# Kernel optimization log

Hardware: AMD Instinct MI355X
Metric: run time of the kernel (lower is better)

## Reference

```python
import jax, jax.numpy as jnp
import numpy as np

S, B, NC = 16, 8, 5
D, H, DH = 256, 16, 16
PS, IMG = 7, 28
P = (IMG // PS) ** 2  # 16 patches
L = 2
PD = PS * PS * 1  # 49
EF, EFT = 4, 0.5
DFT = int(EFT * D)


def layernorm(x, g, b, eps=1e-5):
    m = x.mean(-1, keepdims=True)
    v = ((x - m) ** 2).mean(-1, keepdims=True)
    return (x - m) / jnp.sqrt(v + eps) * g + b


def patchify(x):
    # 's b c (h p1) (w p2) -> s b (h w) (p1 p2 c)'
    s, bb, c, hh, ww = x.shape
    h, w = hh // PS, ww // PS
    x = x.reshape(s, bb, c, h, PS, w, PS)
    x = x.transpose(0, 1, 3, 5, 4, 6, 2)
    return x.reshape(s, bb, h * w, PS * PS * c)


def srwm(x, Wy, Wq, Wk, wb, ln_g, ln_b):
    # Stateful self-referential weight matrix layer (Irie et al. 2022).
    # x: (S, Bn, h*dh); Wy/Wq/Wk: (h, dh, dh); wb: (h, 4, dh)
    s, bn, dim = x.shape
    h, dh = Wy.shape[0], Wy.shape[1]
    xs = x.reshape(s, bn, h, dh)
    bc = lambda W: jnp.broadcast_to(W[None], (bn,) + W.shape)

    def step(carry, xt):
        Wy, Wq, Wk, wb = carry
        y = jnp.einsum('bhij,bhj->bhi', Wy, xt)
        q = jnp.einsum('bhij,bhj->bhi', Wq, xt)
        k = jnp.einsum('bhij,bhj->bhi', Wk, xt)
        beta = jax.nn.sigmoid(jnp.einsum('bhcj,bhj->bhc', wb, xt))  # (Bn,h,4)
        qs = jax.nn.softmax(q, -1)
        ks = jax.nn.softmax(k, -1)
        # old values retrieved with k, target values generated with q
        vy_k = jnp.einsum('bhij,bhj->bhi', Wy, ks)
        vq_k = jnp.einsum('bhij,bhj->bhi', Wq, ks)
        vk_k = jnp.einsum('bhij,bhj->bhi', Wk, ks)
        vb_k = jnp.einsum('bhcj,bhj->bhc', wb, ks)
        vy_q = jax.nn.softmax(jnp.einsum('bhij,bhj->bhi', Wy, qs), -1)
        vq_q = jnp.einsum('bhij,bhj->bhi', Wq, qs)
        vk_q = jnp.einsum('bhij,bhj->bhi', Wk, qs)
        vb_q = jnp.einsum('bhcj,bhj->bhc', wb, qs)
        upd = lambda d, bt: bt[..., None, None] * d[..., None] * ks[..., None, :]
        Wy = Wy + upd(vy_q - vy_k, beta[..., 0])
        Wq = Wq + upd(vq_q - vq_k, beta[..., 1])
        Wk = Wk + upd(vk_q - vk_k, beta[..., 2])
        wb = wb + beta[..., 3, None, None] * (vb_q - vb_k)[..., None] * ks[..., None, :]
        return (Wy, Wq, Wk, wb), y

    _, ys = jax.lax.scan(step, (bc(Wy), bc(Wq), bc(Wk), bc(wb)), xs)
    return layernorm(ys.reshape(s, bn, dim), ln_g, ln_b)


def setup_inputs():
    key = jax.random.key(0)
    ks = iter(jax.random.split(key, 64))
    n = lambda shape, sc: jax.random.normal(next(ks), shape, jnp.float32) * sc
    return dict(
        x=jax.random.normal(next(ks), (S, B, 1, IMG, IMG), jnp.float32),
        fb=jax.random.randint(next(ks), (S, B), 0, NC),
        in_W=n((PD + NC, D), (PD + NC) ** -0.5), in_b=jnp.zeros((D,)),
        tk_Wy=n((L, 1, P, P), P ** -0.5), tk_Wq=n((L, 1, P, P), 0.01 * P ** -0.5),
        tk_Wk=n((L, 1, P, P), P ** -0.5), tk_wb=n((L, 1, 4, P), P ** -0.5),
        tk_lng=jnp.ones((L, P)), tk_lnb=jnp.zeros((L, P)),
        tkm_g=jnp.ones((L, D)), tkm_b=jnp.zeros((L, D)),
        tkm_W1=n((L, P, EF * P), P ** -0.5), tkm_b1=jnp.zeros((L, EF * P)),
        tkm_W2=n((L, EF * P, P), (EF * P) ** -0.5), tkm_b2=jnp.zeros((L, P)),
        ch_Wy=n((L, H, DH, DH), DH ** -0.5), ch_Wq=n((L, H, DH, DH), 0.01 * DH ** -0.5),
        ch_Wk=n((L, H, DH, DH), DH ** -0.5), ch_wb=n((L, H, 4, DH), DH ** -0.5),
        ch_lng=jnp.ones((L, D)), ch_lnb=jnp.zeros((L, D)),
        chm_g=jnp.ones((L, D)), chm_b=jnp.zeros((L, D)),
        chm_W1=n((L, D, DFT), D ** -0.5), chm_b1=jnp.zeros((L, DFT)),
        chm_W2=n((L, DFT, D), DFT ** -0.5), chm_b2=jnp.zeros((L, D)),
        fln_g=jnp.ones((D,)), fln_b=jnp.zeros((D,)),
        o_Wy=n((H, DH, DH), DH ** -0.5), o_Wq=n((H, DH, DH), 0.01 * DH ** -0.5),
        o_Wk=n((H, DH, DH), DH ** -0.5), o_wb=n((H, 4, DH), DH ** -0.5),
        o_lng=jnp.ones((D,)), o_lnb=jnp.zeros((D,)),
        out_W=n((D, NC), D ** -0.5), out_b=jnp.zeros((NC,)),
    )


def reference(x, fb, in_W, in_b, tk_Wy, tk_Wq, tk_Wk, tk_wb, tk_lng, tk_lnb,
              tkm_g, tkm_b, tkm_W1, tkm_b1, tkm_W2, tkm_b2,
              ch_Wy, ch_Wq, ch_Wk, ch_wb, ch_lng, ch_lnb,
              chm_g, chm_b, chm_W1, chm_b1, chm_W2, chm_b2,
              fln_g, fln_b, o_Wy, o_Wq, o_Wk, o_wb, o_lng, o_lnb, out_W, out_b):
    xp = patchify(x)  # (S,B,P,PD)
    emb = jnp.broadcast_to(jax.nn.one_hot(fb, NC)[:, :, None, :], (S, B, P, NC))
    h = jnp.concatenate([xp, emb.astype(xp.dtype)], -1) @ in_W + in_b  # (S,B,P,D)
    for i in range(L):
        # token SRWM: features = patch axis, batch = B*D
        t = jnp.swapaxes(h, -2, -1).reshape(S, B * D, P)
        t = srwm(t, tk_Wy[i], tk_Wq[i], tk_Wk[i], tk_wb[i], tk_lng[i], tk_lnb[i])
        h = jnp.swapaxes(t.reshape(S, B, D, P), -2, -1)
        # token mixer (pre-norm residual, FFN over patch axis)
        hn = jnp.swapaxes(layernorm(h, tkm_g[i], tkm_b[i]), -2, -1)
        hn = jax.nn.gelu(hn @ tkm_W1[i] + tkm_b1[i]) @ tkm_W2[i] + tkm_b2[i]
        h = h + jnp.swapaxes(hn, -2, -1)
        # channel SRWM: features = hidden axis, batch = B*P
        c = srwm(h.reshape(S, B * P, D), ch_Wy[i], ch_Wq[i], ch_Wk[i], ch_wb[i], ch_lng[i], ch_lnb[i])
        h = c.reshape(S, B, P, D)
        # channel mixer
        hn = layernorm(h, chm_g[i], chm_b[i])
        h = h + (jax.nn.gelu(hn @ chm_W1[i] + chm_b1[i]) @ chm_W2[i] + chm_b2[i])
    h = layernorm(h, fln_g, fln_b).mean(-2)  # (S,B,D) mean over patches
    h = srwm(h, o_Wy, o_Wq, o_Wk, o_wb, o_lng, o_lnb)
    return h @ out_W + out_b  # (S,B,NC)
```

## Files before the change

### kernel.cpp

```cpp
#include <hip/hip_runtime.h>
#include <math.h>

constexpr int cS  = 16;
constexpr int cB  = 8;
constexpr int cNC = 5;
constexpr int cD  = 256;
constexpr int cP  = 16;
constexpr int cPD = 49;
#define LEPS 1e-5f
#define GSTR 328

__device__ __forceinline__ float frcp(float x) { return __builtin_amdgcn_rcpf(x); }
__device__ __forceinline__ float sigm(float x) { return frcp(1.0f + __expf(-x)); }
__device__ __forceinline__ float gelu_t(float x) {
  const float z = 1.5957691216057308f * (x + 0.044715f * x * x * x);
  return x * frcp(1.0f + __expf(-z));
}

template<int CTRL>
__device__ __forceinline__ float dpp_mov(float v) {
  return __int_as_float(__builtin_amdgcn_update_dpp(
      0, __float_as_int(v), CTRL, 0xF, 0xF, true));
}
__device__ __forceinline__ float row_sum16(float v) {
  v += dpp_mov<0xB1>(v);
  v += dpp_mov<0x4E>(v);
  v += dpp_mov<0x124>(v);
  v += dpp_mov<0x128>(v);
  return v;
}
__device__ __forceinline__ float wave_sum64(float v) {
  v = row_sum16(v);
  v += __shfl_xor(v, 16, 64);
  v += __shfl_xor(v, 32, 64);
  return v;
}

__device__ __forceinline__ float dot16(const float (&w)[16],
    const float4 a, const float4 b, const float4 c, const float4 d) {
  float s0 = w[0]  * a.x; s0 += w[1]  * a.y; s0 += w[2]  * a.z; s0 += w[3]  * a.w;
  float s1 = w[4]  * b.x; s1 += w[5]  * b.y; s1 += w[6]  * b.z; s1 += w[7]  * b.w;
  float s2 = w[8]  * c.x; s2 += w[9]  * c.y; s2 += w[10] * c.z; s2 += w[11] * c.w;
  float s3 = w[12] * d.x; s3 += w[13] * d.y; s3 += w[14] * d.z; s3 += w[15] * d.w;
  return (s0 + s1) + (s2 + s3);
}

__device__ __forceinline__ void srwm_prestage(
    const float (&xp)[16], float* gl, const int r) {
#pragma unroll
  for (int s = 0; s < 16; ++s) gl[s * 16 + r] = xp[s];
  __builtin_amdgcn_wave_barrier();
}

__device__ __forceinline__ float srwm_step(
    float (&wy)[16], float (&wq)[16], float (&wk)[16], float (&wbr)[16],
    float* gl, const int r, const int s) {
  const float4* xg = (const float4*)(gl + s * 16);
  const float4 xa = xg[0], xb = xg[1], xc = xg[2], xd = xg[3];
  const float y  = dot16(wy,  xa, xb, xc, xd);
  const float q  = dot16(wq,  xa, xb, xc, xd);
  const float k  = dot16(wk,  xa, xb, xc, xd);
  const float bt = dot16(wbr, xa, xb, xc, xd);
  const float bsig = sigm(bt);
  const float eq = __expf(q), ek = __expf(k);
  gl[256 + r] = eq;
  gl[272 + r] = ek;
  gl[288 + r] = bsig;
  __builtin_amdgcn_wave_barrier();
  const float4* g4 = (const float4*)(gl + 256);
  const float4 qa = g4[0], qb = g4[1], qc = g4[2], qd = g4[3];
  const float4 ka = g4[4], kb = g4[5], kc = g4[6], kd = g4[7];
  const float4 bs4 = g4[8];
  const float ay  = dot16(wy,  qa, qb, qc, qd);
  const float vqq = dot16(wq,  qa, qb, qc, qd);
  const float vkq = dot16(wk,  qa, qb, qc, qd);
  const float vbq = dot16(wbr, qa, qb, qc, qd);
  const float vyk = dot16(wy,  ka, kb, kc, kd);
  const float vqk = dot16(wq,  ka, kb, kc, kd);
  const float vkk = dot16(wk,  ka, kb, kc, kd);
  const float vbk = dot16(wbr, ka, kb, kc, kd);
  const float sq = ((qa.x + qa.y) + (qa.z + qa.w)) + ((qb.x + qb.y) + (qb.z + qb.w))
                 + ((qc.x + qc.y) + (qc.z + qc.w)) + ((qd.x + qd.y) + (qd.z + qd.w));
  const float sk = ((ka.x + ka.y) + (ka.z + ka.w)) + ((kb.x + kb.y) + (kb.z + kb.w))
                 + ((kc.x + kc.y) + (kc.z + kc.w)) + ((kd.x + kd.y) + (kd.z + kd.w));
  const float rq = frcp(sq);
  const float rk = frcp(sk);
  const float ea = __expf(ay * rq);
  const float vyq = ea * frcp(row_sum16(ea));
  const float cy = bs4.x * (vyq      - vyk * rk) * rk;
  const float cq = bs4.y * (vqq * rq - vqk * rk) * rk;
  const float ck = bs4.z * (vkq * rq - vkk * rk) * rk;
  const float cb = bs4.w * (vbq * rq - vbk * rk) * rk;
  const float ks[16] = {ka.x, ka.y, ka.z, ka.w, kb.x, kb.y, kb.z, kb.w,
                        kc.x, kc.y, kc.z, kc.w, kd.x, kd.y, kd.z, kd.w};
#pragma unroll
  for (int j = 0; j < 16; ++j) {
    wy[j] += cy * ks[j]; wq[j] += cq * ks[j]; wk[j] += ck * ks[j]; wbr[j] += cb * ks[j];
  }
  return y;
}

__global__ __launch_bounds__(256) void k_embed(const float* __restrict__ x,
                                               const int* __restrict__ fb,
                                               const float* __restrict__ inW,
                                               const float* __restrict__ inb,
                                               float* __restrict__ h) {
  const int blk = blockIdx.x;
  const int p  = blk & 15;
  const int sb = blk >> 4;
  const int ph = p >> 2, pw = p & 3;
  __shared__ float sx[cPD];
  const int t = threadIdx.x;
  if (t < cPD) {
    const int p1 = t / 7, p2 = t % 7;
    sx[t] = x[(size_t)sb * 784 + (ph * 7 + p1) * 28 + (pw * 7 + p2)];
  }
  __syncthreads();
  const int cls = fb[sb];
  float acc = inb[t] + inW[(size_t)(cPD + cls) * cD + t];
#pragma unroll
  for (int j = 0; j < cPD; ++j) acc += sx[j] * inW[(size_t)j * cD + t];
  h[((size_t)sb * cP + p) * cD + t] = acc;
}

__global__ __launch_bounds__(128) void k_tok_srwm(
    float* __restrict__ h, const float* __restrict__ Wy0, const float* __restrict__ Wq0,
    const float* __restrict__ Wk0, const float* __restrict__ wb0,
    const float* __restrict__ lng, const float* __restrict__ lnb) {
  const int t    = threadIdx.x;
  const int lane = t & 63;
  const int w    = t >> 6;
  const int r    = lane & 15;
  const int li   = lane >> 4;
  const int b    = blockIdx.x >> 5;
  const int d    = ((blockIdx.x & 31) << 3) + (w << 2) + li;
  __shared__ __align__(16) float gscr[8][GSTR];
  float* gl = gscr[t >> 4];
  float wy[16], wq[16], wk[16], wbr[16];
#pragma unroll
  for (int j = 0; j < 16; ++j) {
    wy[j]  = Wy0[r * 16 + j];
    wq[j]  = Wq0[r * 16 + j];
    wk[j]  = Wk0[r * 16 + j];
    wbr[j] = wb0[(r & 3) * 16 + j];
  }
  const float gg = lng[r], bb = lnb[r];
  float xp[16];
#pragma unroll
  for (int s = 0; s < 16; ++s)
    xp[s] = h[((size_t)(s * cB + b) * cP + r) * cD + d];
  srwm_prestage(xp, gl, r);
  for (int s = 0; s < cS; ++s) {
    const float y = srwm_step(wy, wq, wk, wbr, gl, r, s);
    const float s1 = row_sum16(y);
    const float s2 = row_sum16(y * y);
    const float m = s1 * 0.0625f;
    const float var = s2 * 0.0625f - m * m;
    h[((size_t)(s * cB + b) * cP + r) * cD + d] = (y - m) * rsqrtf(var + LEPS) * gg + bb;
  }
}

__global__ __launch_bounds__(256) void k_tok_mixer(
    float* __restrict__ h, const float* __restrict__ g, const float* __restrict__ bta,
    const float* __restrict__ W1, const float* __restrict__ b1,
    const float* __restrict__ W2, const float* __restrict__ b2) {
  const int sb = blockIdx.x;
  const int t = threadIdx.x;
  __shared__ float tile[16][256];
  __shared__ float W1s[16 * 64], W2s[64 * 16];
  __shared__ float mean_[16], rstd_[16];
  __shared__ float red[16][17], red2[16][17];
  const size_t base = (size_t)sb * cP * cD;
#pragma unroll
  for (int p = 0; p < 16; ++p) tile[p][t] = h[base + p * 256 + t];
  W1s[t] = W1[t]; W1s[t + 256] = W1[t + 256]; W1s[t + 512] = W1[t + 512]; W1s[t + 768] = W1[t + 768];
  W2s[t] = W2[t]; W2s[t + 256] = W2[t + 256]; W2s[t + 512] = W2[t + 512]; W2s[t + 768] = W2[t + 768];
  __syncthreads();
  const int p = t >> 4, l = t & 15;
  float ps = 0.f, ps2 = 0.f;
#pragma unroll
  for (int k = 0; k < 16; ++k) { const float v = tile[p][l + 16 * k]; ps += v; ps2 += v * v; }
  red[p][l] = ps; red2[p][l] = ps2;
  __syncthreads();
  if (t < 16) {
    float sm = 0.f, s2 = 0.f;
#pragma unroll
    for (int k = 0; k < 16; ++k) { sm += red[t][k]; s2 += red2[t][k]; }
    const float m = sm * (1.f / 256.f);
    mean_[t] = m;
    rstd_[t] = rsqrtf(s2 * (1.f / 256.f) - m * m + LEPS);
  }
  __syncthreads();
  const float gd = g[t], bd = bta[t];
  float v[16], out[16];
#pragma unroll
  for (int pp = 0; pp < 16; ++pp) {
    v[pp] = (tile[pp][t] - mean_[pp]) * rstd_[pp] * gd + bd;
    out[pp] = b2[pp];
  }
  for (int e = 0; e < 64; ++e) {
    float acc = b1[e];
#pragma unroll
    for (int pp = 0; pp < 16; ++pp) acc += v[pp] * W1s[pp * 64 + e];
    const float ge = gelu_t(acc);
#pragma unroll
    for (int pp = 0; pp < 16; ++pp) out[pp] += ge * W2s[e * 16 + pp];
  }
#pragma unroll
  for (int pp = 0; pp < 16; ++pp) h[base + pp * 256 + t] = tile[pp][t] + out[pp];
}

__global__ __launch_bounds__(128) void k_ch_scan(
    const float* __restrict__ h, float* __restrict__ y2,
    const float* __restrict__ Wy0, const float* __restrict__ Wq0,
    const float* __restrict__ Wk0, const float* __restrict__ wb0) {
  const int t  = threadIdx.x;
  const int hg = blockIdx.x & 1;
  const int bp = blockIdx.x >> 1;
  const int hh = (hg << 3) + (t >> 4);
  const int r  = t & 15;
  const int d  = (hg << 7) + t;
  __shared__ __align__(16) float gscr[8][GSTR];
  float* gl = gscr[t >> 4];
  float wy[16], wq[16], wk[16], wbr[16];
#pragma unroll
  for (int j = 0; j < 16; ++j) {
    wy[j]  = Wy0[(hh * 16 + r) * 16 + j];
    wq[j]  = Wq0[(hh * 16 + r) * 16 + j];
    wk[j]  = Wk0[(hh * 16 + r) * 16 + j];
    wbr[j] = wb0[(hh * 4 + (r & 3)) * 16 + j];
  }
  float xp[16];
#pragma unroll
  for (int s = 0; s < 16; ++s)
    xp[s] = h[(size_t)(s * cB * cP + bp) * cD + d];
  srwm_prestage(xp, gl, r);
  for (int s = 0; s < cS; ++s)
    y2[(size_t)(s * cB * cP + bp) * cD + d] = srwm_step(wy, wq, wk, wbr, gl, r, s);
}

__global__ __launch_bounds__(512) void k_ch_ln_mix(
    const float* __restrict__ y2, float* __restrict__ h,
    const float* __restrict__ lng, const float* __restrict__ lnb,
    const float* __restrict__ mg, const float* __restrict__ mb,
    const float* __restrict__ W1, const float* __restrict__ b1,
    const float* __restrict__ W2, const float* __restrict__ b2) {
  const int u = threadIdx.x;
  const int t = u & 255;
  const int jh = u >> 8;
  const int row0 = blockIdx.x * 8;
  __shared__ float yv[8][256];
  __shared__ float lnv[8][256];
  __shared__ float hid[8][128];
  __shared__ float part1[8][128];
  const float4* yp4 = (const float4*)(y2 + (size_t)row0 * cD);
  ((float4*)yv)[u] = yp4[u];
  __syncthreads();
  const int r32 = t >> 5, l = t & 31;
  float4 a0, a1;
  if (jh == 0) {
    const float4 eg0 = ((const float4*)lng)[l * 2];
    const float4 eg1 = ((const float4*)lng)[l * 2 + 1];
    const float4 eb0 = ((const float4*)lnb)[l * 2];
    const float4 eb1 = ((const float4*)lnb)[l * 2 + 1];
    const float4 mg0 = ((const float4*)mg)[l * 2];
    const float4 mg1 = ((const float4*)mg)[l * 2 + 1];
    const float4 mb0 = ((const float4*)mb)[l * 2];
    const float4 mb1 = ((const float4*)mb)[l * 2 + 1];
    const float4 y0 = ((const float4*)yv[r32])[l * 2];
    const float4 y1 = ((const float4*)yv[r32])[l * 2 + 1];
    float s1 = y0.x + y0.y + y0.z + y0.w + y1.x + y1.y + y1.z + y1.w;
    float s2 = y0.x * y0.x + y0.y * y0.y + y0.z * y0.z + y0.w * y0.w +
               y1.x * y1.x + y1.y * y1.y + y1.z * y1.z + y1.w * y1.w;
#pragma unroll
    for (int o = 1; o < 32; o <<= 1) {
      s1 += __shfl_xor(s1, o, 32);
      s2 += __shfl_xor(s2, o, 32);
    }
    const float m1 = s1 * (1.f / 256.f);
    const float rst1 = rsqrtf(s2 * (1.f / 256.f) - m1 * m1 + LEPS);
    a0.x = (y0.x - m1) * rst1 * eg0.x + eb0.x; a0.y = (y0.y - m1) * rst1 * eg0.y + eb0.y;
    a0.z = (y0.z - m1) * rst1 * eg0.z + eb0.z; a0.w = (y0.w - m1) * rst1 * eg0.w + eb0.w;
    a1.x = (y1.x - m1) * rst1 * eg1.x + eb1.x; a1.y = (y1.y - m1) * rst1 * eg1.y + eb1.y;
    a1.z = (y1.z - m1) * rst1 * eg1.z + eb1.z; a1.w = (y1.w - m1) * rst1 * eg1.w + eb1.w;
    float u1 = a0.x + a0.y + a0.z + a0.w + a1.x + a1.y + a1.z + a1.w;
    float u2 = a0.x * a0.x + a0.y * a0.y + a0.z * a0.z + a0.w * a0.w +
               a1.x * a1.x + a1.y * a1.y + a1.z * a1.z + a1.w * a1.w;
#pragma unroll
    for (int o = 1; o < 32; o <<= 1) {
      u1 += __shfl_xor(u1, o, 32);
      u2 += __shfl_xor(u2, o, 32);
    }
    const float m2 = u1 * (1.f / 256.f);
    const float rst2 = rsqrtf(u2 * (1.f / 256.f) - m2 * m2 + LEPS);
    float4 L0, L1;
    L0.x = (a0.x - m2) * rst2 * mg0.x + mb0.x; L0.y = (a0.y - m2) * rst2 * mg0.y + mb0.y;
    L0.z = (a0.z - m2) * rst2 * mg0.z + mb0.z; L0.w = (a0.w - m2) * rst2 * mg0.w + mb0.w;
    L1.x = (a1.x - m2) * rst2 * mg1.x + mb1.x; L1.y = (a1.y - m2) * rst2 * mg1.y + mb1.y;
    L1.z = (a1.z - m2) * rst2 * mg1.z + mb1.z; L1.w = (a1.w - m2) * rst2 * mg1.w + mb1.w;
    ((float4*)lnv[r32])[l * 2]     = L0;
    ((float4*)lnv[r32])[l * 2 + 1] = L1;
  }
  __syncthreads();
  {
    const float4* W1f = (const float4*)W1;
    float4 acc;
    if (jh == 0) acc = ((const float4*)b1)[l];
    else         acc = make_float4(0.f, 0.f, 0.f, 0.f);
    const float4* xrow = (const float4*)lnv[r32];
    for (int j4 = jh * 32; j4 < jh * 32 + 32; ++j4) {
      const float4 xv = xrow[j4];
      const int j = j4 * 4;
      const float4 w0 = W1f[(j + 0) * 32 + l];
      const float4 w1 = W1f[(j + 1) * 32 + l];
      const float4 w2 = W1f[(j + 2) * 32 + l];
      const float4 w3 = W1f[(j + 3) * 32 + l];
      acc.x += xv.x * w0.x + xv.y * w1.x + xv.z * w2.x + xv.w * w3.x;
      acc.y += xv.x * w0.y + xv.y * w1.y + xv.z * w2.y + xv.w * w3.y;
      acc.z += xv.x * w0.z + xv.y * w1.z + xv.z * w2.z + xv.w * w3.z;
      acc.w += xv.x * w0.w + xv.y * w1.w + xv.z * w2.w + xv.w * w3.w;
    }
    if (jh == 1) ((float4*)part1[r32])[l] = acc;
    __syncthreads();
    if (jh == 0) {
      const float4 p = ((const float4*)part1[r32])[l];
      float4 hv;
      hv.x = gelu_t(acc.x + p.x); hv.y = gelu_t(acc.y + p.y);
      hv.z = gelu_t(acc.z + p.z); hv.w = gelu_t(acc.w + p.w);
      ((float4*)hid[r32])[l] = hv;
    }
    __syncthreads();
  }
  {
    const float4* W2f = (const float4*)W2;
    float4 o0, o1;
    if (jh == 0) { o0 = ((const float4*)b2)[l * 2]; o1 = ((const float4*)b2)[l * 2 + 1]; }
    else         { o0 = make_float4(0.f, 0.f, 0.f, 0.f); o1 = o0; }
    const float4* hrow = (const float4*)hid[r32];
    for (int e4 = jh * 16; e4 < jh * 16 + 16; ++e4) {
      const float4 xh = hrow[e4];
      const int e = e4 * 4;
#pragma unroll
      for (int ee = 0; ee < 4; ++ee) {
        const float xv = (ee == 0) ? xh.x : (ee == 1) ? xh.y : (ee == 2) ? xh.z : xh.w;
        const float4 w0 = W2f[(e + ee) * 64 + l * 2];
        const float4 w1 = W2f[(e + ee) * 64 + l * 2 + 1];
        o0.x += xv * w0.x; o0.y += xv * w0.y; o0.z += xv * w0.z; o0.w += xv * w0.w;
        o1.x += xv * w1.x; o1.y += xv * w1.y; o1.z += xv * w1.z; o1.w += xv * w1.w;
      }
    }
    if (jh == 1) {
      ((float4*)yv[r32])[l * 2]     = o0;
      ((float4*)yv[r32])[l * 2 + 1] = o1;
    }
    __syncthreads();
    if (jh == 0) {
      const float4 p0 = ((const float4*)yv[r32])[l * 2];
      const float4 p1 = ((const float4*)yv[r32])[l * 2 + 1];
      o0.x += p0.x + a0.x; o0.y += p0.y + a0.y; o0.z += p0.z + a0.z; o0.w += p0.w + a0.w;
      o1.x += p1.x + a1.x; o1.y += p1.y + a1.y; o1.z += p1.z + a1.z; o1.w += p1.w + a1.w;
      float4* op = (float4*)(h + ((size_t)row0 + r32) * cD);
      op[l * 2]     = o0;
      op[l * 2 + 1] = o1;
    }
  }
}

__global__ __launch_bounds__(256) void k_fln_mean(
    const float* __restrict__ h, const float* __restrict__ gg, const float* __restrict__ bbv,
    float* __restrict__ o) {
  const int sb = blockIdx.x;
  const int t = threadIdx.x;
  const int lane = t & 63, w = t >> 6;
  const float4 g4 = ((const float4*)gg)[lane];
  const float4 b4 = ((const float4*)bbv)[lane];
  float a0 = 0.f, a1 = 0.f, a2 = 0.f, a3 = 0.f;
  for (int pp = 0; pp < 4; ++pp) {
    const int p = w * 4 + pp;
    const float4 v4 = ((const float4*)(h + ((size_t)sb * cP + p) * cD))[lane];
    const float s1 = wave_sum64(v4.x + v4.y + v4.z + v4.w);
    const float s2 = wave_sum64(v4.x * v4.x + v4.y * v4.y + v4.z * v4.z + v4.w * v4.w);
    const float m = s1 * (1.f / 256.f);
    const float rst = rsqrtf(s2 * (1.f / 256.f) - m * m + LEPS);
    a0 += (v4.x - m) * rst * g4.x + b4.x;
    a1 += (v4.y - m) * rst * g4.y + b4.y;
    a2 += (v4.z - m) * rst * g4.z + b4.z;
    a3 += (v4.w - m) * rst * g4.w + b4.w;
  }
  __shared__ float sacc[4][256];
  float4* sp = (float4*)sacc[w];
  sp[lane] = make_float4(a0, a1, a2, a3);
  __syncthreads();
  o[(size_t)sb * cD + t] = (sacc[0][t] + sacc[1][t] + sacc[2][t] + sacc[3][t]) * (1.f / 16.f);
}

__global__ __launch_bounds__(256, 1) void k_out_srwm(
    const float* __restrict__ gin, float* __restrict__ outp,
    const float* __restrict__ Wy0, const float* __restrict__ Wq0,
    const float* __restrict__ Wk0, const float* __restrict__ wb0,
    const float* __restrict__ lng, const float* __restrict__ lnb,
    const float* __restrict__ outW, const float* __restrict__ outb) {
  const int t = threadIdx.x;
  const int lane = t & 63;
  const int w = t >> 6;
  const int hh = t >> 4, r = t & 15;
  const int b = blockIdx.x;
  __shared__ float ymat[16][256];
  __shared__ float gwm[cNC][256];
  __shared__ float GBp[4][10];
  __shared__ float GBs[10];
  __shared__ __align__(16) float gscr[16][GSTR];
  float* gl = gscr[hh];
  float wy[16], wq[16], wk[16], wbr[16];
#pragma unroll
  for (int j = 0; j < 16; ++j) {
    wy[j]  = Wy0[(hh * 16 + r) * 16 + j];
    wq[j]  = Wq0[(hh * 16 + r) * 16 + j];
    wk[j]  = Wk0[(hh * 16 + r) * 16 + j];
    wbr[j] = wb0[(hh * 4 + (r & 3)) * 16 + j];
  }
  {
    const float gg = lng[t], bbl = lnb[t];
    float pg[cNC], pbv[cNC];
#pragma unroll
    for (int c = 0; c < cNC; ++c) {
      const float wv = outW[(size_t)t * cNC + c];
      const float gwv = gg * wv;
      gwm[c][t] = gwv;
      pg[c] = wave_sum64(gwv);
      pbv[c] = wave_sum64(bbl * wv);
    }
    if (lane == 0) {
#pragma unroll
      for (int c = 0; c < cNC; ++c) { GBp[w][c] = pg[c]; GBp[w][5 + c] = pbv[c]; }
    }
    __syncthreads();
    if (t < 10) GBs[t] = GBp[0][t] + GBp[1][t] + GBp[2][t] + GBp[3][t];
    __syncthreads();
  }
  float xp[16];
#pragma unroll
  for (int s = 0; s < 16; ++s) xp[s] = gin[(size_t)(s * cB + b) * cD + t];
  srwm_prestage(xp, gl, r);
  for (int s = 0; s < cS; ++s)
    ymat[s][t] = srwm_step(wy, wq, wk, wbr, gl, r, s);
  __syncthreads();
  for (int k2 = 0; k2 < 4; ++k2) {
    const int sidx = w * 4 + k2;
    const float4 y4 = ((const float4*)ymat[sidx])[lane];
    const float s1 = wave_sum64(y4.x + y4.y + y4.z + y4.w);
    const float s2 = wave_sum64(y4.x * y4.x + y4.y * y4.y + y4.z * y4.z + y4.w * y4.w);
    float S[cNC];
#pragma unroll
    for (int c = 0; c < cNC; ++c) {
      const float4 g4 = ((const float4*)gwm[c])[lane];
      S[c] = wave_sum64(y4.x * g4.x + y4.y * g4.y + y4.z * g4.z + y4.w * g4.w);
    }
    if (lane == 0) {
      const float m = s1 * (1.f / 256.f);
      const float var = s2 * (1.f / 256.f) - m * m;
      const float rst = rsqrtf(var + LEPS);
#pragma unroll
      for (int c = 0; c < cNC; ++c) {
        outp[(size_t)(sidx * cB + b) * cNC + c] =
            outb[c] + rst * S[c] - rst * m * GBs[c] + GBs[5 + c];
      }
    }
  }
}

extern "C" void kernel_launch(void* const* d_in, const int* in_sizes, int n_in,
                              void* d_out, int out_size, void* d_ws, size_t ws_size,
                              hipStream_t stream) {
  const float* x     = (const float*)d_in[0];
  const int*   fb    = (const int*)d_in[1];
  const float* inW   = (const float*)d_in[2];
  const float* inb   = (const float*)d_in[3];
  const float* tkWy  = (const float*)d_in[4];
  const float* tkWq  = (const float*)d_in[5];
  const float* tkWk  = (const float*)d_in[6];
  const float* tkwb  = (const float*)d_in[7];
  const float* tklng = (const float*)d_in[8];
  const float* tklnb = (const float*)d_in[9];
  const float* tkmg  = (const float*)d_in[10];
  const float* tkmb  = (const float*)d_in[11];
  const float* tkmW1 = (const float*)d_in[12];
  const float* tkmb1 = (const float*)d_in[13];
  const float* tkmW2 = (const float*)d_in[14];
  const float* tkmb2 = (const float*)d_in[15];
  const float* chWy  = (const float*)d_in[16];
  const float* chWq  = (const float*)d_in[17];
  const float* chWk  = (const float*)d_in[18];
  const float* chwb  = (const float*)d_in[19];
  const float* chlng = (const float*)d_in[20];
  const float* chlnb = (const float*)d_in[21];
  const float* chmg  = (const float*)d_in[22];
  const float* chmb  = (const float*)d_in[23];
  const float* chmW1 = (const float*)d_in[24];
  const float* chmb1 = (const float*)d_in[25];
  const float* chmW2 = (const float*)d_in[26];
  const float* chmb2 = (const float*)d_in[27];
  const float* flng  = (const float*)d_in[28];
  const float* flnb  = (const float*)d_in[29];
  const float* oWy   = (const float*)d_in[30];
  const float* oWq   = (const float*)d_in[31];
  const float* oWk   = (const float*)d_in[32];
  const float* owb   = (const float*)d_in[33];
  const float* olng  = (const float*)d_in[34];
  const float* olnb  = (const float*)d_in[35];
  const float* outW  = (const float*)d_in[36];
  const float* outb  = (const float*)d_in[37];

  float* h    = (float*)d_ws;
  float* gbuf = h + (size_t)cS * cB * cP * cD;
  float* y2   = gbuf + (size_t)cS * cB * cD;
  float* outp = (float*)d_out;

  k_embed<<<dim3(cS * cB * cP), dim3(256), 0, stream>>>(x, fb, inW, inb, h);
  for (int i = 0; i < 2; ++i) {
    k_tok_srwm<<<dim3(256), dim3(128), 0, stream>>>(
        h, tkWy + i * 256, tkWq + i * 256, tkWk + i * 256, tkwb + i * 64,
        tklng + i * 16, tklnb + i * 16);
    k_tok_mixer<<<dim3(cS * cB), dim3(256), 0, stream>>>(
        h, tkmg + i * 256, tkmb + i * 256, tkmW1 + i * 1024, tkmb1 + i * 64,
        tkmW2 + i * 1024, tkmb2 + i * 16);
    k_ch_scan<<<dim3(cB * cP * 2), dim3(128), 0, stream>>>(
        h, y2, chWy + i * 4096, chWq + i * 4096, chWk + i * 4096, chwb + i * 1024);
    k_ch_ln_mix<<<dim3(cS * cB * cP / 8), dim3(512), 0, stream>>>(
        y2, h, chlng + i * 256, chlnb + i * 256,
        chmg + i * 256, chmb + i * 256, chmW1 + i * 32768, chmb1 + i * 128,
        chmW2 + i * 32768, chmb2 + i * 256);
  }
  k_fln_mean<<<dim3(cS * cB), dim3(256), 0, stream>>>(h, flng, flnb, gbuf);
  k_out_srwm<<<dim3(cB), dim3(256), 0, stream>>>(
      gbuf, outp, oWy, oWq, oWk, owb, olng, olnb, outW, outb);
}
```

Measured before the change: 291.8 us.

## Stage channel-mixer weights through double-buffered shared memory with register prefetch

The channel-mixer kernel now copies W1 and W2 into a 64 KB double-buffered shared-memory tile in four chunks. The next chunk is prefetched into registers while the current one is consumed, instead of every thread reading weights straight from global memory. The goal is to hide global and L2 latency and cut redundant weight loads. The cost is a large LDS footprint, which lowers occupancy, plus several extra block barriers. With only 8 rows per block, staging all the weights may cost more than it saves.

```diff
diff --git a/kernel.cpp b/kernel.cpp
--- a/kernel.cpp
+++ b/kernel.cpp
@@ -253,8 +253,15 @@
   __shared__ float lnv[8][256];
   __shared__ float hid[8][128];
   __shared__ float part1[8][128];
+  __shared__ __align__(16) float wbuf[2][8192];
   const float4* yp4 = (const float4*)(y2 + (size_t)row0 * cD);
   ((float4*)yv)[u] = yp4[u];
+  {
+    const float4* src = (const float4*)W1;
+#pragma unroll
+    for (int kk = 0; kk < 4; ++kk)
+      ((float4*)wbuf[0])[u + kk * 512] = src[u + kk * 512];
+  }
   __syncthreads();
   const int r32 = t >> 5, l = t & 31;
   float4 a0, a1;
@@ -303,22 +310,40 @@
   }
   __syncthreads();
   {
-    const float4* W1f = (const float4*)W1;
     float4 acc;
     if (jh == 0) acc = ((const float4*)b1)[l];
     else         acc = make_float4(0.f, 0.f, 0.f, 0.f);
-    const float4* xrow = (const float4*)lnv[r32];
-    for (int j4 = jh * 32; j4 < jh * 32 + 32; ++j4) {
-      const float4 xv = xrow[j4];
-      const int j = j4 * 4;
-      const float4 w0 = W1f[(j + 0) * 32 + l];
-      const float4 w1 = W1f[(j + 1) * 32 + l];
-      const float4 w2 = W1f[(j + 2) * 32 + l];
-      const float4 w3 = W1f[(j + 3) * 32 + l];
-      acc.x += xv.x * w0.x + xv.y * w1.x + xv.z * w2.x + xv.w * w3.x;
-      acc.y += xv.x * w0.y + xv.y * w1.y + xv.z * w2.y + xv.w * w3.y;
-      acc.z += xv.x * w0.z + xv.y * w1.z + xv.z * w2.z + xv.w * w3.z;
-      acc.w += xv.x * w0.w + xv.y * w1.w + xv.z * w2.w + xv.w * w3.w;
+    const float* xrow = lnv[r32];
+    for (int c = 0; c < 4; ++c) {
+      float4 pf[4];
+      if (c < 3) {
+        const float4* src = (const float4*)W1 + (c + 1) * 2048;
+#pragma unroll
+        for (int kk = 0; kk < 4; ++kk) pf[kk] = src[u + kk * 512];
+      }
+      const float* wc = wbuf[c & 1];
+      const float4* wc4 = (const float4*)wc;
+      const int jbase = c * 64 + jh * 32;
+#pragma unroll
+      for (int j4 = 0; j4 < 8; ++j4) {
+        const int jr = jh * 32 + j4 * 4;
+        const float4 xv = *(const float4*)(xrow + jbase + j4 * 4);
+        const float4 w0 = wc4[(jr + 0) * 32 + l];
+        const float4 w1 = wc4[(jr + 1) * 32 + l];
+        const float4 w2 = wc4[(jr + 2) * 32 + l];
+        const float4 w3 = wc4[(jr + 3) * 32 + l];
+        acc.x += xv.x * w0.x + xv.y * w1.x + xv.z * w2.x + xv.w * w3.x;
+        acc.y += xv.x * w0.y + xv.y * w1.y + xv.z * w2.y + xv.w * w3.y;
+        acc.z += xv.x * w0.z + xv.y * w1.z + xv.z * w2.z + xv.w * w3.z;
+        acc.w += xv.x * w0.w + xv.y * w1.w + xv.z * w2.w + xv.w * w3.w;
+      }
+      if (c < 3) {
+        __syncthreads();
+        float4* dst = (float4*)wbuf[(c + 1) & 1];
+#pragma unroll
+        for (int kk = 0; kk < 4; ++kk) dst[u + kk * 512] = pf[kk];
+        __syncthreads();
+      }
     }
     if (jh == 1) ((float4*)part1[r32])[l] = acc;
     __syncthreads();
@@ -332,21 +357,40 @@
     __syncthreads();
   }
   {
-    const float4* W2f = (const float4*)W2;
     float4 o0, o1;
     if (jh == 0) { o0 = ((const float4*)b2)[l * 2]; o1 = ((const float4*)b2)[l * 2 + 1]; }
     else         { o0 = make_float4(0.f, 0.f, 0.f, 0.f); o1 = o0; }
-    const float4* hrow = (const float4*)hid[r32];
-    for (int e4 = jh * 16; e4 < jh * 16 + 16; ++e4) {
-      const float4 xh = hrow[e4];
-      const int e = e4 * 4;
-#pragma unroll
-      for (int ee = 0; ee < 4; ++ee) {
-        const float xv = (ee == 0) ? xh.x : (ee == 1) ? xh.y : (ee == 2) ? xh.z : xh.w;
-        const float4 w0 = W2f[(e + ee) * 64 + l * 2];
-        const float4 w1 = W2f[(e + ee) * 64 + l * 2 + 1];
+    {
+      const float4* src = (const float4*)W2;
+#pragma unroll
+      for (int kk = 0; kk < 4; ++kk) ((float4*)wbuf[0])[u + kk * 512] = src[u + kk * 512];
+    }
+    __syncthreads();
+    const float* hrow = hid[r32];
+    for (int c = 0; c < 4; ++c) {
+      float4 pf[4];
+      if (c < 3) {
+        const float4* src = (const float4*)W2 + (c + 1) * 2048;
+#pragma unroll
+        for (int kk = 0; kk < 4; ++kk) pf[kk] = src[u + kk * 512];
+      }
+      const float4* wc4 = (const float4*)wbuf[c & 1];
+      const int ebase = c * 32 + jh * 16;
+#pragma unroll
+      for (int ee = 0; ee < 16; ++ee) {
+        const int er = jh * 16 + ee;
+        const float xv = hrow[ebase + ee];
+        const float4 w0 = wc4[er * 64 + l * 2];
+        const float4 w1 = wc4[er * 64 + l * 2 + 1];
         o0.x += xv * w0.x; o0.y += xv * w0.y; o0.z += xv * w0.z; o0.w += xv * w0.w;
         o1.x += xv * w1.x; o1.y += xv * w1.y; o1.z += xv * w1.z; o1.w += xv * w1.w;
+      }
+      if (c < 3) {
+        __syncthreads();
+        float4* dst = (float4*)wbuf[(c + 1) & 1];
+#pragma unroll
+        for (int kk = 0; kk < 4; ++kk) dst[u + kk * 512] = pf[kk];
+        __syncthreads();
       }
     }
     if (jh == 1) {
```

Measured after the change: 315.2 us. +8.0%, slower.
